# Performance work log

Hardware: AMD Instinct MI355X
Metric: run time of the kernel (lower is better)

The kernel has to match this reference:

```python
import jax, jax.numpy as jnp
import numpy as np

B, C, CW = 64, 862, 512
F_BINS = CW // 2 + 1          # 257 rfft bins -> embedding in_features
D_MODEL, N_HEADS, D_FF, N_LAYERS = 256, 16, 512, 3
EPS = 1e-5


def setup_inputs() -> dict:
    key = jax.random.key(0)
    ks = jax.random.split(key, 12)
    s = 0.02
    return {
        'x_re': jax.random.normal(ks[0], (B, C, F_BINS), jnp.float32),
        'x_im': jax.random.normal(ks[1], (B, C, F_BINS), jnp.float32),
        # complex embedding Linear(F_BINS, D_MODEL): weight [D_MODEL, F_BINS], bias [D_MODEL]
        'emb_Wre': jax.random.normal(ks[2], (D_MODEL, F_BINS), jnp.float32) * s,
        'emb_Wim': jax.random.normal(ks[3], (D_MODEL, F_BINS), jnp.float32) * s,
        'emb_bre': jax.random.normal(ks[4], (D_MODEL,), jnp.float32) * s,
        'emb_bim': jax.random.normal(ks[5], (D_MODEL,), jnp.float32) * s,
        # per-layer FFN weights (stacked over layers)
        'W1': jax.random.normal(ks[6], (N_LAYERS, D_FF, D_MODEL), jnp.float32) * s,
        'b1': jnp.zeros((N_LAYERS, D_FF), jnp.float32),
        'W2': jax.random.normal(ks[7], (N_LAYERS, D_MODEL, D_FF), jnp.float32) * s,
        'b2': jnp.zeros((N_LAYERS, D_MODEL), jnp.float32),
        # per-layer BatchNorm affine params (attn norm and ffn norm)
        'gamma1': jnp.ones((N_LAYERS, D_MODEL), jnp.float32),
        'beta1': jnp.zeros((N_LAYERS, D_MODEL), jnp.float32),
        'gamma2': jnp.ones((N_LAYERS, D_MODEL), jnp.float32),
        'beta2': jnp.zeros((N_LAYERS, D_MODEL), jnp.float32),
    }


def _batchnorm(x, g, b):
    # Transpose(1,2) + BatchNorm1d(d_model) + Transpose(1,2): normalize each
    # feature (last axis) over (batch, seq) with batch statistics (training mode).
    m = x.mean(axis=(0, 1))
    v = x.var(axis=(0, 1))  # biased, matching torch normalization
    return (x - m) * jax.lax.rsqrt(v + EPS) * g + b


def _encoder_layer(y, Wff1, bff1, Wff2, bff2, g1, be1, g2, be2):
    # y: [2b, c, d] -- real half stacked over imag half along dim 0
    scale = float(D_MODEL // N_HEADS) ** -0.5
    b = y.shape[0] // 2
    # _MultiheadAttention: q = src, k = flip(src, dims=[1,2]), v = src (no projections applied)
    k = jnp.flip(y, axis=(1, 2))
    q_re, q_im = y[:b], y[b:]
    k_re, k_im = k[:b], k[b:]
    v_re = y[:b]
    v_im = y[:b]  # faithful to source: both halves use v[:bs//2]
    asr = scale * (q_re * k_re - q_im * k_im)
    asi = scale * (q_re * k_im - q_im * k_re)  # minus, as written in source
    o_re = asr * v_re - asi * v_im
    o_im = asr * v_im + asi * v_re
    out = jnp.concatenate([o_re, o_im], axis=0)  # [2b, c, d]
    # transpose(1,2).contiguous().view(bs, -1, d_model): a data shuffle, kept faithfully
    out = jnp.swapaxes(out, 1, 2).reshape(out.shape[0], out.shape[1], out.shape[2])
    src = y + out                       # residual (dropout = 0)
    src = _batchnorm(src, g1, be1)      # post-norm (pre_norm=False)
    ff = jnp.einsum('bcd,fd->bcf', src, Wff1) + bff1
    ff = jax.nn.gelu(ff, approximate=False)
    ff = jnp.einsum('bcf,df->bcd', ff, Wff2) + bff2
    src = src + ff
    src = _batchnorm(src, g2, be2)
    return src


def reference(x_re, x_im, emb_Wre, emb_Wim, emb_bre, emb_bim,
              W1, b1, W2, b2, gamma1, beta1, gamma2, beta2):
    # complex Linear embedding: (x_re + i x_im) @ (Wre + i Wim)^T + (bre + i bim)
    y_re = x_re @ emb_Wre.T - x_im @ emb_Wim.T + emb_bre
    y_im = x_re @ emb_Wim.T + x_im @ emb_Wre.T + emb_bim
    y = jnp.concatenate([y_re, y_im], axis=0)  # [2b, c, d_model]
    for i in range(N_LAYERS):
        y = _encoder_layer(y, W1[i], b1[i], W2[i], b2[i],
                           gamma1[i], beta1[i], gamma2[i], beta2[i])
    b = x_re.shape[0]
    # torch.view_as_complex(stack([y[:b], y[b:]], -1)) -> return real/imag stacked
    return jnp.stack([y[:b], y[b:]], axis=-1)  # [b, c, d_model, 2]
```

## Files before the change

kernel.cpp:

```cpp
#include <hip/hip_runtime.h>
#include <hip/hip_bf16.h>
#include <math.h>

#define BB   64
#define CC   862
#define FB   257
#define DM   256
#define DFF  512
#define NIMG 128
#define ROWS_RE (BB*CC)
#define ROWS_ALL (NIMG*CC)
#define NELEM ((long)ROWS_ALL*DM)

typedef __bf16 bf16x8 __attribute__((ext_vector_type(8)));
typedef float  f32x4  __attribute__((ext_vector_type(4)));

__global__ __launch_bounds__(256) void k_wcvt(const float* __restrict__ W1,
                                              const float* __restrict__ W2,
                                              __bf16* __restrict__ W1b,
                                              __bf16* __restrict__ W2b) {
  long i = ((long)blockIdx.x * 256 + threadIdx.x) * 4;
  const long N1 = 3L * DFF * DM;
  const float* src;
  __bf16* dst;
  if (i < N1) { src = W1 + i; dst = W1b + i; }
  else        { src = W2 + (i - N1); dst = W2b + (i - N1); }
  float4 x = *(const float4*)src;
  dst[0] = (__bf16)x.x; dst[1] = (__bf16)x.y;
  dst[2] = (__bf16)x.z; dst[3] = (__bf16)x.w;
}

__global__ void k_ident(float* ss) {
  int d = threadIdx.x;
  ss[d] = 1.0f;
  ss[DM + d] = 0.0f;
}

#define KE 544
#define PE 552

__global__ __launch_bounds__(256) void k_wemb(const float* __restrict__ Wre,
                                              const float* __restrict__ Wim,
                                              __bf16* __restrict__ Wb) {
  int n = blockIdx.x;
  int d = n & 255;
  bool im = (n >= 256);
  const float* Wa = im ? Wim : Wre;
  const float* Wc = im ? Wre : Wim;
  float sgn = im ? 1.0f : -1.0f;
  for (int k = threadIdx.x; k < KE; k += 256) {
    float v;
    if (k < 257)      v = Wa[(long)d * FB + k];
    else if (k < 514) v = sgn * Wc[(long)d * FB + (k - 257)];
    else              v = 0.0f;
    Wb[(long)n * KE + k] = (__bf16)v;
  }
}

__global__ __launch_bounds__(256, 4) void k_embm(
    const float* __restrict__ xr, const float* __restrict__ xi,
    const __bf16* __restrict__ Wb,
    const float* __restrict__ bre, const float* __restrict__ bim,
    float* __restrict__ A) {
  __shared__ __bf16 sA[32 * PE];
  int t = threadIdx.x;
  int lane = t & 63;
  int w = t >> 6;
  int half = lane >> 4;
  int l16 = lane & 15;
  long row0 = (long)blockIdx.x * 32;

  for (int idx = t; idx < 32 * 30; idx += 256) {
    int r = idx / 30, j = idx - r * 30;
    sA[r * PE + 514 + j] = (__bf16)0.f;
  }
  for (int idx = t; idx < 32 * 257; idx += 256) {
    int r = idx / 257, f = idx - r * 257;
    long g = (row0 + r) * FB + f;
    sA[r * PE + f]       = (__bf16)xr[g];
    sA[r * PE + 257 + f] = (__bf16)xi[g];
  }
  __syncthreads();

  int n0 = w * 128;
  f32x4 acc[2][8];
#pragma unroll
  for (int mt = 0; mt < 2; mt++)
#pragma unroll
    for (int j = 0; j < 8; j++) acc[mt][j] = (f32x4){0.f, 0.f, 0.f, 0.f};

#pragma unroll 1
  for (int kt = 0; kt < 17; kt++) {
    int kb = kt * 32 + half * 8;
    bf16x8 a[2];
#pragma unroll
    for (int mt = 0; mt < 2; mt++)
      a[mt] = *(const bf16x8*)&sA[(mt * 16 + l16) * PE + kb];
#pragma unroll
    for (int j = 0; j < 8; j++) {
      bf16x8 bfr = *(const bf16x8*)&Wb[(long)(n0 + j * 16 + l16) * KE + kb];
#pragma unroll
      for (int mt = 0; mt < 2; mt++)
        acc[mt][j] = __builtin_amdgcn_mfma_f32_16x16x32_bf16(a[mt], bfr, acc[mt][j], 0, 0, 0);
    }
  }

#pragma unroll
  for (int j = 0; j < 8; j++) {
    int n = n0 + j * 16 + l16;
    int d = n & 255;
    float bv = (n < 256) ? bre[d] : bim[d];
    long rbase = (n < 256) ? 0L : (long)ROWS_RE;
#pragma unroll
    for (int mt = 0; mt < 2; mt++)
#pragma unroll
      for (int r = 0; r < 4; r++) {
        int m = mt * 16 + half * 4 + r;
        A[(row0 + m + rbase) * DM + d] = acc[mt][j][r] + bv;
      }
  }
}

__global__ __launch_bounds__(256) void k_attn(const float* __restrict__ A,
                                              const float* __restrict__ ss,
                                              float* __restrict__ T) {
  __shared__ float ore[32][33];
  __shared__ float oim[32][33];
  __shared__ float ssc[256];
  __shared__ float ssh[256];
  int tx = threadIdx.x;
  int ty = threadIdx.y;
  int t = ty * 32 + tx;
  ssc[t] = ss[t];
  ssh[t] = ss[DM + t];
  __syncthreads();

  int c0 = blockIdx.x * 32;
  int d0 = blockIdx.y * 32;
  int b  = blockIdx.z;
  const long base_re = (long)b * CC * DM;
  const long base_im = (long)(b + BB) * CC * DM;
  int d = d0 + tx;
  int kd = DM - 1 - d;
  float scq = ssc[d], shq = ssh[d];
  float sck = ssc[kd], shk = ssh[kd];
#pragma unroll
  for (int q = 0; q < 4; q++) {
    int cl = ty + 8 * q;
    int c = c0 + cl;
    if (c < CC) {
      float qr = fmaf(A[base_re + (long)c * DM + d], scq, shq);
      float qi = fmaf(A[base_im + (long)c * DM + d], scq, shq);
      float kr = fmaf(A[base_re + (long)(CC - 1 - c) * DM + kd], sck, shk);
      float ki = fmaf(A[base_im + (long)(CC - 1 - c) * DM + kd], sck, shk);
      float asr = 0.25f * (qr * kr - qi * ki);
      float asi = 0.25f * (qr * ki - qi * kr);
      ore[cl][tx] = (asr - asi) * qr;
      oim[cl][tx] = (asr + asi) * qr;
    }
  }
  __syncthreads();
#pragma unroll
  for (int q = 0; q < 4; q++) {
    int dl = ty + 8 * q;
    int dd = d0 + dl;
    int c = c0 + tx;
    if (c < CC) {
      long flat = (long)dd * CC + c;
      int dp = (int)(flat & 255);
      float sc = ssc[dp], sh = ssh[dp];
      T[base_re + flat] = fmaf(A[base_re + flat], sc, sh) + ore[tx][dl];
      T[base_im + flat] = fmaf(A[base_im + flat], sc, sh) + oim[tx][dl];
    }
  }
}

__global__ void k_zero(double* s) { s[threadIdx.x] = 0.0; }

__global__ __launch_bounds__(256) void k_bnstats(const float* __restrict__ P,
                                                 double* __restrict__ stats) {
  int d = threadIdx.x;
  long row0 = (long)blockIdx.x * 128;
  double s = 0.0, s2 = 0.0;
  for (int r = 0; r < 128; r++) {
    float x = P[(row0 + r) * DM + d];
    s += (double)x;
    s2 += (double)x * (double)x;
  }
  atomicAdd(&stats[d], s);
  atomicAdd(&stats[DM + d], s2);
}

__global__ void k_finalize(double* __restrict__ stats,
                           const float* __restrict__ g, const float* __restrict__ be,
                           float* __restrict__ ss) {
  int d = threadIdx.x;
  double n = (double)ROWS_ALL;
  double m = stats[d] / n;
  double v = stats[DM + d] / n - m * m;
  float inv = (float)(1.0 / sqrt(v + 1e-5));
  float sc = g[d] * inv;
  ss[d] = sc;
  ss[DM + d] = be[d] - (float)m * sc;
  stats[d] = 0.0;
  stats[DM + d] = 0.0;
}

__global__ __launch_bounds__(256) void k_bnfinal(const float* __restrict__ A,
                                                 const float* __restrict__ ss,
                                                 float* __restrict__ out) {
  long gid = (long)blockIdx.x * 256 + threadIdx.x;
  int d = (int)(gid & 255);
  long bc = gid >> 8;
  float sc = ss[d], sh = ss[DM + d];
  float re = A[bc * DM + d];
  float im = A[(bc + (long)ROWS_RE) * DM + d];
  float2 o;
  o.x = fmaf(re, sc, sh);
  o.y = fmaf(im, sc, sh);
  ((float2*)out)[gid] = o;
}

#define PS2 264
#define PHH 264

__global__ __launch_bounds__(512, 4) void k_ffm(
    const float* __restrict__ P, const float* __restrict__ ss,
    const __bf16* __restrict__ W1b, const float* __restrict__ b1,
    const __bf16* __restrict__ W2b, const float* __restrict__ b2,
    float* __restrict__ Out, double* __restrict__ stats) {
  __shared__ __bf16 sS[64 * PS2];
  __shared__ __bf16 sH[64 * PHH];
  int t = threadIdx.x;
  int lane = t & 63;
  int w = t >> 6;
  int half = lane >> 4;
  int l16 = lane & 15;
  long row0 = (long)blockIdx.x * 64;

  {
    const float4* Pv = (const float4*)(P + row0 * DM);
    const float4* scv = (const float4*)ss;
    const float4* shv = (const float4*)(ss + DM);
#pragma unroll
    for (int i = 0; i < 8; i++) {
      int v = t + i * 512;
      int r = v >> 6, k4 = v & 63;
      float4 x = Pv[(long)r * 64 + k4];
      float4 sc = scv[k4];
      float4 sh = shv[k4];
      x.x = fmaf(x.x, sc.x, sh.x);
      x.y = fmaf(x.y, sc.y, sh.y);
      x.z = fmaf(x.z, sc.z, sh.z);
      x.w = fmaf(x.w, sc.w, sh.w);
      __bf16* dst = &sS[r * PS2 + k4 * 4];
      dst[0] = (__bf16)x.x; dst[1] = (__bf16)x.y;
      dst[2] = (__bf16)x.z; dst[3] = (__bf16)x.w;
    }
  }
  __syncthreads();

  int n2 = w * 32;
  f32x4 acc2[4][2];
#pragma unroll
  for (int mt = 0; mt < 4; mt++)
#pragma unroll
    for (int j = 0; j < 2; j++) acc2[mt][j] = (f32x4){0.f, 0.f, 0.f, 0.f};

#pragma unroll 1
  for (int hf = 0; hf < 2; hf++) {
    if (hf == 1) __syncthreads();

    f32x4 acc[4][2];
#pragma unroll
    for (int mt = 0; mt < 4; mt++)
#pragma unroll
      for (int j = 0; j < 2; j++) acc[mt][j] = (f32x4){0.f, 0.f, 0.f, 0.f};

#pragma unroll 2
    for (int kt = 0; kt < 8; kt++) {
      int kb = kt * 32 + half * 8;
      bf16x8 a[4];
#pragma unroll
      for (int mt = 0; mt < 4; mt++)
        a[mt] = *(const bf16x8*)&sS[(mt * 16 + l16) * PS2 + kb];
#pragma unroll
      for (int j = 0; j < 2; j++) {
        bf16x8 bfr = *(const bf16x8*)&W1b[(long)(hf * 256 + w * 32 + j * 16 + l16) * DM + kb];
#pragma unroll
        for (int mt = 0; mt < 4; mt++)
          acc[mt][j] = __builtin_amdgcn_mfma_f32_16x16x32_bf16(a[mt], bfr, acc[mt][j], 0, 0, 0);
      }
    }

#pragma unroll
    for (int j = 0; j < 2; j++) {
      int fl = w * 32 + j * 16 + l16;
      float b1v = b1[hf * 256 + fl];
#pragma unroll
      for (int mt = 0; mt < 4; mt++)
#pragma unroll
        for (int r = 0; r < 4; r++) {
          float x = acc[mt][j][r] + b1v;
          float u = x * (0.7978845608f + 0.0356774081f * x * x);
          float g = x / (1.0f + __expf(-2.0f * u));
          int m = mt * 16 + half * 4 + r;
          sH[m * PHH + fl] = (__bf16)g;
        }
    }
    __syncthreads();

#pragma unroll 2
    for (int kt = 0; kt < 8; kt++) {
      int kb = kt * 32 + half * 8;
      bf16x8 a[4];
#pragma unroll
      for (int mt = 0; mt < 4; mt++)
        a[mt] = *(const bf16x8*)&sH[(mt * 16 + l16) * PHH + kb];
#pragma unroll
      for (int j = 0; j < 2; j++) {
        bf16x8 bfr = *(const bf16x8*)&W2b[(long)(n2 + j * 16 + l16) * DFF + hf * 256 + kb];
#pragma unroll
        for (int mt = 0; mt < 4; mt++)
          acc2[mt][j] = __builtin_amdgcn_mfma_f32_16x16x32_bf16(a[mt], bfr, acc2[mt][j], 0, 0, 0);
      }
    }
  }

  {
#pragma unroll
    for (int j = 0; j < 2; j++) {
      int d = n2 + j * 16 + l16;
      float b2v = b2[d];
      float sc = ss[d], sh = ss[DM + d];
      float s = 0.f, s2 = 0.f;
#pragma unroll
      for (int mt = 0; mt < 4; mt++)
#pragma unroll
        for (int r = 0; r < 4; r++) {
          int m = mt * 16 + half * 4 + r;
          long idx = (row0 + m) * DM + d;
          float vv = fmaf(P[idx], sc, sh) + acc2[mt][j][r] + b2v;
          Out[idx] = vv;
          s += vv;
          s2 += vv * vv;
        }
      s  += __shfl_xor(s, 16);  s  += __shfl_xor(s, 32);
      s2 += __shfl_xor(s2, 16); s2 += __shfl_xor(s2, 32);
      if (half == 0) {
        atomicAdd(&stats[d], (double)s);
        atomicAdd(&stats[DM + d], (double)s2);
      }
    }
  }
}

extern "C" void kernel_launch(void* const* d_in, const int* in_sizes, int n_in,
                              void* d_out, int out_size, void* d_ws, size_t ws_size,
                              hipStream_t stream) {
  const float* xr  = (const float*)d_in[0];
  const float* xi  = (const float*)d_in[1];
  const float* Wre = (const float*)d_in[2];
  const float* Wim = (const float*)d_in[3];
  const float* bre = (const float*)d_in[4];
  const float* bim = (const float*)d_in[5];
  const float* W1  = (const float*)d_in[6];
  const float* b1  = (const float*)d_in[7];
  const float* W2  = (const float*)d_in[8];
  const float* b2  = (const float*)d_in[9];
  const float* g1  = (const float*)d_in[10];
  const float* be1 = (const float*)d_in[11];
  const float* g2  = (const float*)d_in[12];
  const float* be2 = (const float*)d_in[13];

  float* A = (float*)d_ws;
  double* stats = (double*)((char*)d_ws + (size_t)NELEM * 4);
  float* ss = (float*)(stats + 512);
  __bf16* W1b = (__bf16*)(ss + 512);
  __bf16* W2b = W1b + 3L * DFF * DM;
  float* T = (float*)d_out;
  __bf16* Wb = (__bf16*)d_out;

  k_wemb<<<512, 256, 0, stream>>>(Wre, Wim, Wb);
  k_wcvt<<<768, 256, 0, stream>>>(W1, W2, W1b, W2b);
  k_zero<<<1, 512, 0, stream>>>(stats);
  k_ident<<<1, 256, 0, stream>>>(ss);
  k_embm<<<ROWS_RE / 32, 256, 0, stream>>>(xr, xi, Wb, bre, bim, A);

  for (int l = 0; l < 3; l++) {
    k_attn<<<dim3(27, 8, 64), dim3(32, 8), 0, stream>>>(A, ss, T);
    k_bnstats<<<862, 256, 0, stream>>>(T, stats);
    k_finalize<<<1, 256, 0, stream>>>(stats, g1 + l * DM, be1 + l * DM, ss);
    k_ffm<<<ROWS_ALL / 64, 512, 0, stream>>>(T, ss,
                                             W1b + (long)l * DFF * DM, b1 + l * DFF,
                                             W2b + (long)l * DFF * DM, b2 + l * DM,
                                             A, stats);
    k_finalize<<<1, 256, 0, stream>>>(stats, g2 + l * DM, be2 + l * DM, ss);
    if (l == 2) {
      k_bnfinal<<<ROWS_RE * DM / 256, 256, 0, stream>>>(A, ss, (float*)d_out);
    }
  }
}
```

Measured before the change: 1.222 ms.

## Fuse BatchNorm statistics into attention kernel and drop separate stats pass

The attention kernel now loops over all eight d-tiles per block and accumulates per-feature sum and sum-of-squares in shared memory via LDS atomics, then pushes them to global double stats. This removes the separate k_bnstats kernel, which re-read the whole activation tensor. In exchange the attention grid shrinks by 8x, so each block does more serial work with lower parallelism, and it adds contended shared-memory float atomics plus float-precision partial sums. The FFN MFMA loops are also unrolled by 4 instead of 2.

After: 1.369 ms. 1.12x slower.

```diff
diff --git a/kernel.cpp b/kernel.cpp
--- a/kernel.cpp
+++ b/kernel.cpp
@@ -123,73 +123,76 @@
 
 __global__ __launch_bounds__(256) void k_attn(const float* __restrict__ A,
                                               const float* __restrict__ ss,
-                                              float* __restrict__ T) {
+                                              float* __restrict__ T,
+                                              double* __restrict__ stats) {
   __shared__ float ore[32][33];
   __shared__ float oim[32][33];
   __shared__ float ssc[256];
   __shared__ float ssh[256];
+  __shared__ float lsum[256];
+  __shared__ float lsum2[256];
   int tx = threadIdx.x;
   int ty = threadIdx.y;
   int t = ty * 32 + tx;
   ssc[t] = ss[t];
   ssh[t] = ss[DM + t];
+  lsum[t] = 0.f;
+  lsum2[t] = 0.f;
   __syncthreads();
 
   int c0 = blockIdx.x * 32;
-  int d0 = blockIdx.y * 32;
-  int b  = blockIdx.z;
+  int b  = blockIdx.y;
   const long base_re = (long)b * CC * DM;
   const long base_im = (long)(b + BB) * CC * DM;
-  int d = d0 + tx;
-  int kd = DM - 1 - d;
-  float scq = ssc[d], shq = ssh[d];
-  float sck = ssc[kd], shk = ssh[kd];
-#pragma unroll
-  for (int q = 0; q < 4; q++) {
-    int cl = ty + 8 * q;
-    int c = c0 + cl;
-    if (c < CC) {
-      float qr = fmaf(A[base_re + (long)c * DM + d], scq, shq);
-      float qi = fmaf(A[base_im + (long)c * DM + d], scq, shq);
-      float kr = fmaf(A[base_re + (long)(CC - 1 - c) * DM + kd], sck, shk);
-      float ki = fmaf(A[base_im + (long)(CC - 1 - c) * DM + kd], sck, shk);
-      float asr = 0.25f * (qr * kr - qi * ki);
-      float asi = 0.25f * (qr * ki - qi * kr);
-      ore[cl][tx] = (asr - asi) * qr;
-      oim[cl][tx] = (asr + asi) * qr;
+
+#pragma unroll 1
+  for (int dt = 0; dt < 8; dt++) {
+    if (dt > 0) __syncthreads();
+    int d0 = dt * 32;
+    int d = d0 + tx;
+    int kd = DM - 1 - d;
+    float scq = ssc[d], shq = ssh[d];
+    float sck = ssc[kd], shk = ssh[kd];
+#pragma unroll
+    for (int q = 0; q < 4; q++) {
+      int cl = ty + 8 * q;
+      int c = c0 + cl;
+      if (c < CC) {
+        float qr = fmaf(A[base_re + (long)c * DM + d], scq, shq);
+        float qi = fmaf(A[base_im + (long)c * DM + d], scq, shq);
+        float kr = fmaf(A[base_re + (long)(CC - 1 - c) * DM + kd], sck, shk);
+        float ki = fmaf(A[base_im + (long)(CC - 1 - c) * DM + kd], sck, shk);
+        float asr = 0.25f * (qr * kr - qi * ki);
+        float asi = 0.25f * (qr * ki - qi * kr);
+        ore[cl][tx] = (asr - asi) * qr;
+        oim[cl][tx] = (asr + asi) * qr;
+      }
+    }
+    __syncthreads();
+#pragma unroll
+    for (int q = 0; q < 4; q++) {
+      int dl = ty + 8 * q;
+      int dd = d0 + dl;
+      int c = c0 + tx;
+      if (c < CC) {
+        long flat = (long)dd * CC + c;
+        int dp = (int)(flat & 255);
+        float sc = ssc[dp], sh = ssh[dp];
+        float vre = fmaf(A[base_re + flat], sc, sh) + ore[tx][dl];
+        float vim = fmaf(A[base_im + flat], sc, sh) + oim[tx][dl];
+        T[base_re + flat] = vre;
+        T[base_im + flat] = vim;
+        atomicAdd(&lsum[dp], vre + vim);
+        atomicAdd(&lsum2[dp], vre * vre + vim * vim);
+      }
     }
   }
   __syncthreads();
-#pragma unroll
-  for (int q = 0; q < 4; q++) {
-    int dl = ty + 8 * q;
-    int dd = d0 + dl;
-    int c = c0 + tx;
-    if (c < CC) {
-      long flat = (long)dd * CC + c;
-      int dp = (int)(flat & 255);
-      float sc = ssc[dp], sh = ssh[dp];
-      T[base_re + flat] = fmaf(A[base_re + flat], sc, sh) + ore[tx][dl];
-      T[base_im + flat] = fmaf(A[base_im + flat], sc, sh) + oim[tx][dl];
-    }
-  }
+  atomicAdd(&stats[t], (double)lsum[t]);
+  atomicAdd(&stats[DM + t], (double)lsum2[t]);
 }
 
 __global__ void k_zero(double* s) { s[threadIdx.x] = 0.0; }
-
-__global__ __launch_bounds__(256) void k_bnstats(const float* __restrict__ P,
-                                                 double* __restrict__ stats) {
-  int d = threadIdx.x;
-  long row0 = (long)blockIdx.x * 128;
-  double s = 0.0, s2 = 0.0;
-  for (int r = 0; r < 128; r++) {
-    float x = P[(row0 + r) * DM + d];
-    s += (double)x;
-    s2 += (double)x * (double)x;
-  }
-  atomicAdd(&stats[d], s);
-  atomicAdd(&stats[DM + d], s2);
-}
 
 __global__ void k_finalize(double* __restrict__ stats,
                            const float* __restrict__ g, const float* __restrict__ be,
@@ -277,7 +280,7 @@
 #pragma unroll
       for (int j = 0; j < 2; j++) acc[mt][j] = (f32x4){0.f, 0.f, 0.f, 0.f};
 
-#pragma unroll 2
+#pragma unroll 4
     for (int kt = 0; kt < 8; kt++) {
       int kb = kt * 32 + half * 8;
       bf16x8 a[4];
@@ -310,7 +313,7 @@
     }
     __syncthreads();
 
-#pragma unroll 2
+#pragma unroll 4
     for (int kt = 0; kt < 8; kt++) {
       int kb = kt * 32 + half * 8;
       bf16x8 a[4];
@@ -388,8 +391,7 @@
   k_embm<<<ROWS_RE / 32, 256, 0, stream>>>(xr, xi, Wb, bre, bim, A);
 
   for (int l = 0; l < 3; l++) {
-    k_attn<<<dim3(27, 8, 64), dim3(32, 8), 0, stream>>>(A, ss, T);
-    k_bnstats<<<862, 256, 0, stream>>>(T, stats);
+    k_attn<<<dim3(27, 64), dim3(32, 8), 0, stream>>>(A, ss, T, stats);
     k_finalize<<<1, 256, 0, stream>>>(stats, g1 + l * DM, be1 + l * DM, ss);
     k_ffm<<<ROWS_ALL / 64, 512, 0, stream>>>(T, ss,
                                              W1b + (long)l * DFF * DM, b1 + l * DFF,
```
